# Optimization experiments

Measured on AMD Instinct MI355X. Metric: run time of the kernel, lower is better.

Reference implementation:

```python
import jax, jax.numpy as jnp
import numpy as np
from jax import lax

DIM = 64
NUM_EXPERTS = 6
TOP_K = 2
B, H, W = 8, 128, 128
DN = ('NCHW', 'OIHW', 'NCHW')


def setup_inputs() -> dict:
    key = jax.random.key(0)
    ks = jax.random.split(key, 8)
    s_in = 1.0 / np.sqrt(DIM * 9)
    s_r = 1.0 / np.sqrt(DIM)
    return {
        'x': jax.random.normal(ks[0], (B, DIM, H, W), jnp.float32),
        'router_w': jax.random.normal(ks[1], (NUM_EXPERTS, DIM), jnp.float32) * s_r,
        'router_b': jnp.zeros((NUM_EXPERTS,), jnp.float32),
        'expert_bias': jnp.zeros((NUM_EXPERTS,), jnp.float32),
        'w1': jax.random.normal(ks[2], (NUM_EXPERTS, DIM, DIM, 3, 3), jnp.float32) * s_in,
        'b1': jnp.zeros((NUM_EXPERTS, DIM), jnp.float32),
        'w2': jax.random.normal(ks[3], (NUM_EXPERTS, DIM, DIM, 3, 3), jnp.float32) * s_in,
        'b2': jnp.zeros((NUM_EXPERTS, DIM), jnp.float32),
    }


def reference(x, router_w, router_b, expert_bias, w1, b1, w2, b2):
    # ---- router: global avg pool -> linear -> clamp -> +bias -> softmax ----
    pooled = x.mean(axis=(2, 3))                               # [B, C]
    logits = pooled @ router_w.T + router_b                    # [B, E]
    logits = jnp.clip(logits, -10.0, 10.0) + expert_bias[None, :]
    probs = jnp.clip(jax.nn.softmax(logits, axis=1), 1e-6, 1.0)
    top_v, top_i = lax.top_k(probs, TOP_K)                     # [B, K]
    top_v = top_v / (top_v.sum(axis=1, keepdims=True) + 1e-8)
    # per-sample combine weight for each expert: sum of top-k probs routed to it
    w_be = (jax.nn.one_hot(top_i, NUM_EXPERTS, dtype=x.dtype) * top_v[..., None]).sum(axis=1)  # [B, E]

    # ---- experts: Conv3x3 -> GELU -> Conv3x3, vmapped over expert dim ----
    def expert(w1e, b1e, w2e, b2e):
        h = lax.conv_general_dilated(x, w1e, (1, 1), 'SAME', dimension_numbers=DN)
        h = jax.nn.gelu(h + b1e[None, :, None, None])
        h = lax.conv_general_dilated(h, w2e, (1, 1), 'SAME', dimension_numbers=DN)
        return h + b2e[None, :, None, None]

    ys = jax.vmap(expert)(w1, b1, w2, b2)                      # [E, B, C, H, W]
    out = jnp.einsum('be,ebchw->bchw', w_be, ys)
    return out, jnp.zeros((), x.dtype)
```

## Files before the change

kernel.cpp:

```cpp
#include <hip/hip_runtime.h>
#include <hip/hip_bf16.h>
#include <cstdint>

typedef __attribute__((ext_vector_type(8))) short sh8;
typedef __attribute__((ext_vector_type(16))) float f32x16;
typedef unsigned short ushort_t;

#define HH 128
#define WW 128
#define HWSZ (HH*WW)
#define PW 130
#define PW64 (PW*64)
#define IMGSZ ((size_t)PW*PW*64)
#define WBEXP 36864

#define SCOLS 34
#define ROWB (SCOLS*128)
#define TRT 4
#define SRT 6
#define CHT (SRT*SCOLS*8)

typedef __attribute__((address_space(1))) const void gvoid_t;
typedef __attribute__((address_space(3))) void lvoid_t;

__device__ __forceinline__ float gelu_fast(float x) {
    float m = x * __builtin_fmaf(x * x, -0.10294323f, -2.30220805f);
    return x * __builtin_amdgcn_rcpf(1.0f + __builtin_amdgcn_exp2f(m));
}
__device__ __forceinline__ ushort_t f2b(float f) {
    __hip_bfloat16 h = __float2bfloat16(f);
    return *reinterpret_cast<ushort_t*>(&h);
}
__device__ __forceinline__ unsigned pack2(float a, float b) {
    return (unsigned)f2b(a) | ((unsigned)f2b(b) << 16);
}
__device__ __forceinline__ f32x16 mfma_bf16(sh8 a, sh8 b, f32x16 c) {
    return __builtin_amdgcn_mfma_f32_32x32x16_bf16(a, b, c, 0, 0, 0);
}

__device__ __forceinline__ void stage_gll(const ushort_t* __restrict__ imgRow,
                                          char* smem, int w0, int tid) {
#pragma unroll
    for (int it = 0; it < 7; ++it) {
        int idx = tid + it * 256;
        if (idx < CHT) {
            int row = idx / (SCOLS * 8);
            int rem = idx - row * (SCOLS * 8);
            int col = rem >> 3;
            int ch  = (rem & 7) ^ (col & 7);
            const ushort_t* src = imgRow + (size_t)row * PW64 + (size_t)(w0 + col) * 64 + ch * 8;
            __builtin_amdgcn_global_load_lds((gvoid_t*)src, (lvoid_t*)(smem + idx * 16),
                                             16, 0, 0);
        }
    }
}

__device__ __forceinline__ void conv_phase1(const char* sm, const ushort_t* wt_,
                                            int row, int l31, int lh,
                                            f32x16& acc0, f32x16& acc1, int dc) {
    sh8 wf[8];
#pragma unroll
    for (int kc = 0; kc < 4; ++kc) {
        wf[kc * 2]     = *reinterpret_cast<const sh8*>(wt_ + kc * 1024);
        wf[kc * 2 + 1] = *reinterpret_cast<const sh8*>(wt_ + kc * 1024 + 512);
    }
    __builtin_amdgcn_sched_barrier(0);
    const int colb = (dc + l31) * 128;
    const int swz = ((dc + l31) & 7) << 4;
#pragma unroll
    for (int kc = 0; kc < 4; ++kc) {
        sh8 a = *reinterpret_cast<const sh8*>(sm + row * ROWB + ((colb + (kc * 2 + lh) * 16) ^ swz));
        acc0 = mfma_bf16(wf[kc * 2], a, acc0);
        acc1 = mfma_bf16(wf[kc * 2 + 1], a, acc1);
    }
}

__global__ __launch_bounds__(64) void router_kernel(const float* __restrict__ pooled,
                                                    const float* __restrict__ rw,
                                                    const float* __restrict__ rb,
                                                    const float* __restrict__ eb,
                                                    const float* __restrict__ b2,
                                                    int* __restrict__ topi,
                                                    float* __restrict__ topw,
                                                    float* __restrict__ bsum,
                                                    float* __restrict__ outz) {
    __shared__ int sti[16];
    __shared__ float stw[16];
    int b = threadIdx.x;
    if (b == 8) outz[(size_t)8 * 64 * HWSZ] = 0.f;
    if (b < 8) {
        float lg[6];
        for (int e = 0; e < 6; ++e) {
            float s = 0.f;
            for (int c = 0; c < 64; ++c) s += pooled[b * 64 + c] * rw[e * 64 + c];
            s = s * (1.0f / (float)HWSZ) + rb[e];
            lg[e] = fminf(fmaxf(s, -10.f), 10.f) + eb[e];
        }
        float m = lg[0];
        for (int e = 1; e < 6; ++e) m = fmaxf(m, lg[e]);
        float den = 0.f, pr[6];
        for (int e = 0; e < 6; ++e) { pr[e] = expf(lg[e] - m); den += pr[e]; }
        float inv = 1.0f / den;
        for (int e = 0; e < 6; ++e) pr[e] = fminf(fmaxf(pr[e] * inv, 1e-6f), 1.0f);
        int i0 = 0; float v0 = pr[0];
        for (int e = 1; e < 6; ++e) if (pr[e] > v0) { v0 = pr[e]; i0 = e; }
        int i1 = -1; float v1 = -1.f;
        for (int e = 0; e < 6; ++e) { if (e == i0) continue; if (pr[e] > v1) { v1 = pr[e]; i1 = e; } }
        float s2 = v0 + v1 + 1e-8f;
        topi[b * 2 + 0] = i0; topi[b * 2 + 1] = i1;
        topw[b * 2 + 0] = v0 / s2; topw[b * 2 + 1] = v1 / s2;
        sti[b * 2 + 0] = i0; sti[b * 2 + 1] = i1;
        stw[b * 2 + 0] = v0 / s2; stw[b * 2 + 1] = v1 / s2;
    }
    __syncthreads();
    for (int i = threadIdx.x; i < 512; i += 64) {
        int bb = i >> 6, c = i & 63;
        bsum[i] = stw[bb * 2] * b2[sti[bb * 2] * 64 + c] +
                  stw[bb * 2 + 1] * b2[sti[bb * 2 + 1] * 64 + c];
    }
}

__global__ __launch_bounds__(256) void convx_kernel(const float* __restrict__ x,
                                                    ushort_t* __restrict__ xp,
                                                    float* __restrict__ pooled) {
    __shared__ ushort_t lt[128][72];
    int b = blockIdx.x >> 7, h = blockIdx.x & 127;
    int tid = threadIdx.x;
#pragma unroll
    for (int k = 0; k < 8; ++k) {
        int idx = tid + k * 256;
        int ci = idx >> 5, wg = idx & 31;
        float4 v = *reinterpret_cast<const float4*>(
            x + ((size_t)b * 64 + ci) * HWSZ + (size_t)h * WW + wg * 4);
        lt[wg * 4 + 0][ci] = f2b(v.x);
        lt[wg * 4 + 1][ci] = f2b(v.y);
        lt[wg * 4 + 2][ci] = f2b(v.z);
        lt[wg * 4 + 3][ci] = f2b(v.w);
        float s4 = (v.x + v.y) + (v.z + v.w);
#pragma unroll
        for (int m = 16; m > 0; m >>= 1) s4 += __shfl_xor(s4, m, 64);
        if ((tid & 31) == 0) atomicAdd(pooled + b * 64 + ci, s4);
    }
    __syncthreads();
    int w = tid >> 1, half = tid & 1;
    const int4* src = reinterpret_cast<const int4*>(&lt[w][half * 32]);
    int4 a0 = src[0], a1 = src[1], a2 = src[2], a3 = src[3];
    int4* dst = reinterpret_cast<int4*>(
        xp + (((size_t)b * PW + (h + 1)) * PW + (w + 1)) * 64 + half * 32);
    dst[0] = a0; dst[1] = a1; dst[2] = a2; dst[3] = a3;
}

__global__ __launch_bounds__(256) void prep_kernel(const float* __restrict__ w1,
                                                   const float* __restrict__ w2,
                                                   const int* __restrict__ topi,
                                                   const float* __restrict__ topw,
                                                   ushort_t* __restrict__ wb1f,
                                                   ushort_t* __restrict__ wb2f,
                                                   ushort_t* __restrict__ xp,
                                                   ushort_t* __restrict__ hp) {
    int blk = blockIdx.x;
    int tid = threadIdx.x;
    if (blk < 54) {
        int e = blk / 9, t = blk - e * 9;
        for (int idx = tid; idx < 4096; idx += 256) {
            int kc = idx >> 10, n = (idx >> 9) & 1, l = (idx >> 3) & 63, j = idx & 7;
            int co = n * 32 + (l & 31);
            int ci = kc * 16 + (l >> 5) * 8 + j;
            wb1f[(size_t)e * WBEXP + t * 4096 + idx] =
                f2b(w1[(((size_t)e * 64 + co) * 64 + ci) * 9 + t]);
        }
    } else if (blk < 198) {
        int q = blk - 54;
        int bs = q / 9, t = q - bs * 9;
        int e = topi[bs];
        float cw = topw[bs];
        for (int idx = tid; idx < 4096; idx += 256) {
            int kc = idx >> 10, n = (idx >> 9) & 1, l = (idx >> 3) & 63, j = idx & 7;
            int co = n * 32 + (l & 31);
            int ci = kc * 16 + (l >> 5) * 8 + j;
            wb2f[(size_t)bs * WBEXP + t * 4096 + idx] =
                f2b(cw * w2[(((size_t)e * 64 + co) * 64 + ci) * 9 + t]);
        }
    } else {
        int img = blk - 198;
        ushort_t* p = (img < 8) ? (xp + (size_t)img * IMGSZ)
                                : (hp + (size_t)(img - 8) * IMGSZ);
        int4 z = make_int4(0, 0, 0, 0);
        for (int i = tid; i < 1040; i += 256) {
            reinterpret_cast<int4*>(p)[i] = z;
            reinterpret_cast<int4*>(p + (size_t)129 * PW64)[i] = z;
        }
        for (int i = tid; i < 128 * 8; i += 256) {
            int row = 1 + (i >> 3), j = i & 7;
            reinterpret_cast<int4*>(p + (size_t)row * PW64)[j] = z;
            reinterpret_cast<int4*>(p + ((size_t)row * PW + 129) * 64)[j] = z;
        }
    }
}

__global__ __launch_bounds__(256) void conv1_mfma(const ushort_t* __restrict__ xp,
                                                  const ushort_t* __restrict__ wb1f,
                                                  const float* __restrict__ b1,
                                                  const int* __restrict__ topi,
                                                  ushort_t* __restrict__ hp,
                                                  int nslots, int slot0) {
    __shared__ char smem[CHT * 16];
    const int z = blockIdx.z;
    const int b = z / nslots, sl = z - b * nslots, s = slot0 + sl;
    const int e = topi[b * 2 + s];
    const int tid = threadIdx.x, l = tid & 63, wid = tid >> 6;
    const int l31 = l & 31, lh = l >> 5;
    const int ht = blockIdx.x >> 2, wt = blockIdx.x & 3;
    const int h0 = ht * TRT, w0 = wt * 32;
    const int row0 = wid;

    stage_gll(xp + (size_t)b * IMGSZ + (size_t)h0 * PW64, smem, w0, tid);

    const ushort_t* wB = wb1f + (size_t)e * WBEXP + l * 8;
    f32x16 acc0, acc1;
#pragma unroll
    for (int k2 = 0; k2 < 16; ++k2) { acc0[k2] = 0.f; acc1[k2] = 0.f; }
    __syncthreads();

#pragma unroll
    for (int dr = 0; dr < 3; ++dr)
#pragma unroll
        for (int dc = 0; dc < 3; ++dc)
            conv_phase1(smem, wB + (dr * 3 + dc) * 4096, row0 + dr, l31, lh, acc0, acc1, dc);

    float4 bq[2][4];
#pragma unroll
    for (int n = 0; n < 2; ++n)
#pragma unroll
        for (int g = 0; g < 4; ++g)
            bq[n][g] = *reinterpret_cast<const float4*>(b1 + e * 64 + n * 32 + g * 8 + 4 * lh);
    const size_t pbase = (size_t)(sl * 8 + b) * IMGSZ +
                         (size_t)(h0 + row0 + 1) * PW64 + (size_t)(w0 + l31 + 1) * 64;
#pragma unroll
    for (int n = 0; n < 2; ++n) {
        f32x16 a = n ? acc1 : acc0;
#pragma unroll
        for (int g = 0; g < 4; ++g) {
            float v0 = gelu_fast(a[g * 4 + 0] + bq[n][g].x);
            float v1 = gelu_fast(a[g * 4 + 1] + bq[n][g].y);
            float v2 = gelu_fast(a[g * 4 + 2] + bq[n][g].z);
            float v3 = gelu_fast(a[g * 4 + 3] + bq[n][g].w);
            uint2 u; u.x = pack2(v0, v1); u.y = pack2(v2, v3);
            *reinterpret_cast<uint2*>(hp + pbase + n * 32 + g * 8 + 4 * lh) = u;
        }
    }
}

template <int NS>
__global__ __launch_bounds__(256) void conv2_mfma(const ushort_t* __restrict__ hp,
                                                  const ushort_t* __restrict__ wb2f,
                                                  const float* __restrict__ bsum,
                                                  float* __restrict__ outF,
                                                  int s0, int addmode) {
    __shared__ char smem[2][CHT * 16];
    const int b = blockIdx.z;
    const int tid = threadIdx.x, l = tid & 63, wid = tid >> 6;
    const int l31 = l & 31, lh = l >> 5;
    const int ht = blockIdx.x >> 2, wt = blockIdx.x & 3;
    const int h0 = ht * TRT, w0 = wt * 32;
    const int row0 = wid;

    stage_gll(hp + (size_t)b * IMGSZ + (size_t)h0 * PW64, smem[0], w0, tid);

    f32x16 acc0, acc1;
#pragma unroll
    for (int k2 = 0; k2 < 16; ++k2) { acc0[k2] = 0.f; acc1[k2] = 0.f; }
    __syncthreads();

    if (NS == 2)
        stage_gll(hp + (size_t)(8 + b) * IMGSZ + (size_t)h0 * PW64, smem[1], w0, tid);

    {
        const ushort_t* wB = wb2f + (size_t)(b * 2 + s0) * WBEXP + l * 8;
#pragma unroll
        for (int dr = 0; dr < 3; ++dr)
#pragma unroll
            for (int dc = 0; dc < 3; ++dc)
                conv_phase1(smem[0], wB + (dr * 3 + dc) * 4096, row0 + dr, l31, lh, acc0, acc1, dc);
    }
    if (NS == 2) {
        __syncthreads();
        const ushort_t* wB = wb2f + (size_t)(b * 2 + s0 + 1) * WBEXP + l * 8;
#pragma unroll
        for (int dr = 0; dr < 3; ++dr)
#pragma unroll
            for (int dc = 0; dc < 3; ++dc)
                conv_phase1(smem[1], wB + (dr * 3 + dc) * 4096, row0 + dr, l31, lh, acc0, acc1, dc);
    }

    __syncthreads();
    float* lt = reinterpret_cast<float*>(smem[0]) + wid * 1056;
    float4 bq[2][4];
#pragma unroll
    for (int n = 0; n < 2; ++n)
#pragma unroll
        for (int g = 0; g < 4; ++g)
            bq[n][g] = addmode ? make_float4(0.f, 0.f, 0.f, 0.f)
                               : *reinterpret_cast<const float4*>(bsum + b * 64 + n * 32 + g * 8 + 4 * lh);
    const int h = h0 + row0;
#pragma unroll
    for (int n = 0; n < 2; ++n) {
        f32x16 a = n ? acc1 : acc0;
#pragma unroll
        for (int r = 0; r < 16; ++r) {
            int co = (r & 3) + 8 * (r >> 2) + 4 * lh;
            float bv = (r & 3) == 0 ? bq[n][r >> 2].x : (r & 3) == 1 ? bq[n][r >> 2].y
                     : (r & 3) == 2 ? bq[n][r >> 2].z : bq[n][r >> 2].w;
            lt[l31 * 33 + co] = a[r] + bv;
        }
        const int q = lh, co = l31;
        const size_t ob = ((size_t)(b * 64 + n * 32 + co)) * HWSZ + (size_t)h * WW + w0 + q * 16;
#pragma unroll
        for (int v = 0; v < 4; ++v) {
            float o0 = lt[(q * 16 + v * 4 + 0) * 33 + co];
            float o1 = lt[(q * 16 + v * 4 + 1) * 33 + co];
            float o2 = lt[(q * 16 + v * 4 + 2) * 33 + co];
            float o3 = lt[(q * 16 + v * 4 + 3) * 33 + co];
            float4* dst = reinterpret_cast<float4*>(outF + ob + v * 4);
            if (addmode) {
                float4 pv = *dst;
                o0 += pv.x; o1 += pv.y; o2 += pv.z; o3 += pv.w;
            }
            float4 o; o.x = o0; o.y = o1; o.z = o2; o.w = o3;
            *dst = o;
        }
    }
}

extern "C" void kernel_launch(void* const* d_in, const int* in_sizes, int n_in,
                              void* d_out, int out_size, void* d_ws, size_t ws_size,
                              hipStream_t stream) {
    const float* x  = (const float*)d_in[0];
    const float* rw = (const float*)d_in[1];
    const float* rb = (const float*)d_in[2];
    const float* eb = (const float*)d_in[3];
    const float* w1 = (const float*)d_in[4];
    const float* b1 = (const float*)d_in[5];
    const float* w2 = (const float*)d_in[6];
    const float* b2 = (const float*)d_in[7];
    float* out = (float*)d_out;

    char* ws = (char*)d_ws;
    float*    pooled = (float*)(ws + 0);
    int*      topi   = (int*)(ws + 2048);
    float*    topw   = (float*)(ws + 2112);
    float*    bsum   = (float*)(ws + 2176);
    ushort_t* wb1f   = (ushort_t*)(ws + 4352);
    ushort_t* wb2f   = (ushort_t*)(ws + 446720);
    ushort_t* xp     = (ushort_t*)(ws + 1626368);
    ushort_t* hp     = (ushort_t*)(ws + 18931968);

    const bool two = ws_size >= 53543168ull;

    hipMemsetAsync(pooled, 0, 512 * sizeof(float), stream);
    hipLaunchKernelGGL(convx_kernel, dim3(1024), dim3(256), 0, stream, x, xp, pooled);
    hipLaunchKernelGGL(router_kernel, dim3(1), dim3(64), 0, stream,
                       pooled, rw, rb, eb, b2, topi, topw, bsum, out);
    hipLaunchKernelGGL(prep_kernel, dim3(198 + 8 + (two ? 16 : 8)), dim3(256), 0, stream,
                       w1, w2, topi, topw, wb1f, wb2f, xp, hp);

    if (two) {
        hipLaunchKernelGGL(conv1_mfma, dim3(128, 1, 16), dim3(256), 0, stream,
                           xp, wb1f, b1, topi, hp, 2, 0);
        hipLaunchKernelGGL((conv2_mfma<2>), dim3(128, 1, 8), dim3(256), 0, stream,
                           hp, wb2f, bsum, out, 0, 0);
    } else {
        hipLaunchKernelGGL(conv1_mfma, dim3(128, 1, 8), dim3(256), 0, stream,
                           xp, wb1f, b1, topi, hp, 1, 0);
        hipLaunchKernelGGL((conv2_mfma<1>), dim3(128, 1, 8), dim3(256), 0, stream,
                           hp, wb2f, bsum, out, 0, 0);
        hipLaunchKernelGGL(conv1_mfma, dim3(128, 1, 8), dim3(256), 0, stream,
                           xp, wb1f, b1, topi, hp, 1, 1);
        hipLaunchKernelGGL((conv2_mfma<1>), dim3(128, 1, 8), dim3(256), 0, stream,
                           hp, wb2f, bsum, out, 1, 1);
    }
}
```

Baseline: 211.2 us.

## Halve conv tile rows and split output channels across waves

Each block now covers 2 output rows instead of 4, and each wave computes one 32-channel half of the output instead of both halves. This doubles the grid and cuts per-wave accumulator registers and LDS footprint, which should raise occupancy. The two-slot conv2 now reuses a single LDS buffer and restages sequentially with extra barriers, which drops the earlier prefetch overlap. Smaller tiles also increase halo reload overhead, since each block now loads 4 staged rows for 2 output rows rather than 6 for 4.

```diff
diff --git a/kernel.cpp b/kernel.cpp
--- a/kernel.cpp
+++ b/kernel.cpp
@@ -16,8 +16,8 @@
 
 #define SCOLS 34
 #define ROWB (SCOLS*128)
-#define TRT 4
-#define SRT 6
+#define TRT 2
+#define SRT 4
 #define CHT (SRT*SCOLS*8)
 
 typedef __attribute__((address_space(1))) const void gvoid_t;
@@ -41,7 +41,7 @@
 __device__ __forceinline__ void stage_gll(const ushort_t* __restrict__ imgRow,
                                           char* smem, int w0, int tid) {
 #pragma unroll
-    for (int it = 0; it < 7; ++it) {
+    for (int it = 0; it < 5; ++it) {
         int idx = tid + it * 256;
         if (idx < CHT) {
             int row = idx / (SCOLS * 8);
@@ -57,21 +57,18 @@
 
 __device__ __forceinline__ void conv_phase1(const char* sm, const ushort_t* wt_,
                                             int row, int l31, int lh,
-                                            f32x16& acc0, f32x16& acc1, int dc) {
-    sh8 wf[8];
-#pragma unroll
-    for (int kc = 0; kc < 4; ++kc) {
-        wf[kc * 2]     = *reinterpret_cast<const sh8*>(wt_ + kc * 1024);
-        wf[kc * 2 + 1] = *reinterpret_cast<const sh8*>(wt_ + kc * 1024 + 512);
-    }
+                                            f32x16& acc, int dc) {
+    sh8 wf[4];
+#pragma unroll
+    for (int kc = 0; kc < 4; ++kc)
+        wf[kc] = *reinterpret_cast<const sh8*>(wt_ + kc * 1024);
     __builtin_amdgcn_sched_barrier(0);
     const int colb = (dc + l31) * 128;
     const int swz = ((dc + l31) & 7) << 4;
 #pragma unroll
     for (int kc = 0; kc < 4; ++kc) {
         sh8 a = *reinterpret_cast<const sh8*>(sm + row * ROWB + ((colb + (kc * 2 + lh) * 16) ^ swz));
-        acc0 = mfma_bf16(wf[kc * 2], a, acc0);
-        acc1 = mfma_bf16(wf[kc * 2 + 1], a, acc1);
+        acc = mfma_bf16(wf[kc], a, acc);
     }
 }
 
@@ -212,42 +209,37 @@
     const int l31 = l & 31, lh = l >> 5;
     const int ht = blockIdx.x >> 2, wt = blockIdx.x & 3;
     const int h0 = ht * TRT, w0 = wt * 32;
-    const int row0 = wid;
+    const int row0 = wid >> 1;
+    const int n = wid & 1;
 
     stage_gll(xp + (size_t)b * IMGSZ + (size_t)h0 * PW64, smem, w0, tid);
 
-    const ushort_t* wB = wb1f + (size_t)e * WBEXP + l * 8;
-    f32x16 acc0, acc1;
-#pragma unroll
-    for (int k2 = 0; k2 < 16; ++k2) { acc0[k2] = 0.f; acc1[k2] = 0.f; }
+    const ushort_t* wB = wb1f + (size_t)e * WBEXP + n * 512 + l * 8;
+    f32x16 acc;
+#pragma unroll
+    for (int k2 = 0; k2 < 16; ++k2) acc[k2] = 0.f;
     __syncthreads();
 
 #pragma unroll
     for (int dr = 0; dr < 3; ++dr)
 #pragma unroll
         for (int dc = 0; dc < 3; ++dc)
-            conv_phase1(smem, wB + (dr * 3 + dc) * 4096, row0 + dr, l31, lh, acc0, acc1, dc);
-
-    float4 bq[2][4];
-#pragma unroll
-    for (int n = 0; n < 2; ++n)
-#pragma unroll
-        for (int g = 0; g < 4; ++g)
-            bq[n][g] = *reinterpret_cast<const float4*>(b1 + e * 64 + n * 32 + g * 8 + 4 * lh);
+            conv_phase1(smem, wB + (dr * 3 + dc) * 4096, row0 + dr, l31, lh, acc, dc);
+
+    float4 bq[4];
+#pragma unroll
+    for (int g = 0; g < 4; ++g)
+        bq[g] = *reinterpret_cast<const float4*>(b1 + e * 64 + n * 32 + g * 8 + 4 * lh);
     const size_t pbase = (size_t)(sl * 8 + b) * IMGSZ +
                          (size_t)(h0 + row0 + 1) * PW64 + (size_t)(w0 + l31 + 1) * 64;
 #pragma unroll
-    for (int n = 0; n < 2; ++n) {
-        f32x16 a = n ? acc1 : acc0;
-#pragma unroll
-        for (int g = 0; g < 4; ++g) {
-            float v0 = gelu_fast(a[g * 4 + 0] + bq[n][g].x);
-            float v1 = gelu_fast(a[g * 4 + 1] + bq[n][g].y);
-            float v2 = gelu_fast(a[g * 4 + 2] + bq[n][g].z);
-            float v3 = gelu_fast(a[g * 4 + 3] + bq[n][g].w);
-            uint2 u; u.x = pack2(v0, v1); u.y = pack2(v2, v3);
-            *reinterpret_cast<uint2*>(hp + pbase + n * 32 + g * 8 + 4 * lh) = u;
-        }
+    for (int g = 0; g < 4; ++g) {
+        float v0 = gelu_fast(acc[g * 4 + 0] + bq[g].x);
+        float v1 = gelu_fast(acc[g * 4 + 1] + bq[g].y);
+        float v2 = gelu_fast(acc[g * 4 + 2] + bq[g].z);
+        float v3 = gelu_fast(acc[g * 4 + 3] + bq[g].w);
+        uint2 u; u.x = pack2(v0, v1); u.y = pack2(v2, v3);
+        *reinterpret_cast<uint2*>(hp + pbase + n * 32 + g * 8 + 4 * lh) = u;
     }
 }
 
@@ -257,78 +249,72 @@
                                                   const float* __restrict__ bsum,
                                                   float* __restrict__ outF,
                                                   int s0, int addmode) {
-    __shared__ char smem[2][CHT * 16];
+    __shared__ char smem[CHT * 16];
     const int b = blockIdx.z;
     const int tid = threadIdx.x, l = tid & 63, wid = tid >> 6;
     const int l31 = l & 31, lh = l >> 5;
     const int ht = blockIdx.x >> 2, wt = blockIdx.x & 3;
     const int h0 = ht * TRT, w0 = wt * 32;
-    const int row0 = wid;
-
-    stage_gll(hp + (size_t)b * IMGSZ + (size_t)h0 * PW64, smem[0], w0, tid);
-
-    f32x16 acc0, acc1;
-#pragma unroll
-    for (int k2 = 0; k2 < 16; ++k2) { acc0[k2] = 0.f; acc1[k2] = 0.f; }
-    __syncthreads();
-
-    if (NS == 2)
-        stage_gll(hp + (size_t)(8 + b) * IMGSZ + (size_t)h0 * PW64, smem[1], w0, tid);
+    const int row0 = wid >> 1;
+    const int n = wid & 1;
+
+    stage_gll(hp + (size_t)b * IMGSZ + (size_t)h0 * PW64, smem, w0, tid);
+
+    f32x16 acc;
+#pragma unroll
+    for (int k2 = 0; k2 < 16; ++k2) acc[k2] = 0.f;
+    __syncthreads();
 
     {
-        const ushort_t* wB = wb2f + (size_t)(b * 2 + s0) * WBEXP + l * 8;
+        const ushort_t* wB = wb2f + (size_t)(b * 2 + s0) * WBEXP + n * 512 + l * 8;
 #pragma unroll
         for (int dr = 0; dr < 3; ++dr)
 #pragma unroll
             for (int dc = 0; dc < 3; ++dc)
-                conv_phase1(smem[0], wB + (dr * 3 + dc) * 4096, row0 + dr, l31, lh, acc0, acc1, dc);
+                conv_phase1(smem, wB + (dr * 3 + dc) * 4096, row0 + dr, l31, lh, acc, dc);
     }
     if (NS == 2) {
         __syncthreads();
-        const ushort_t* wB = wb2f + (size_t)(b * 2 + s0 + 1) * WBEXP + l * 8;
+        stage_gll(hp + (size_t)(8 + b) * IMGSZ + (size_t)h0 * PW64, smem, w0, tid);
+        __syncthreads();
+        const ushort_t* wB = wb2f + (size_t)(b * 2 + s0 + 1) * WBEXP + n * 512 + l * 8;
 #pragma unroll
         for (int dr = 0; dr < 3; ++dr)
 #pragma unroll
             for (int dc = 0; dc < 3; ++dc)
-                conv_phase1(smem[1], wB + (dr * 3 + dc) * 4096, row0 + dr, l31, lh, acc0, acc1, dc);
-    }
-
-    __syncthreads();
-    float* lt = reinterpret_cast<float*>(smem[0]) + wid * 1056;
-    float4 bq[2][4];
-#pragma unroll
-    for (int n = 0; n < 2; ++n)
-#pragma unroll
-        for (int g = 0; g < 4; ++g)
-            bq[n][g] = addmode ? make_float4(0.f, 0.f, 0.f, 0.f)
-                               : *reinterpret_cast<const float4*>(bsum + b * 64 + n * 32 + g * 8 + 4 * lh);
+                conv_phase1(smem, wB + (dr * 3 + dc) * 4096, row0 + dr, l31, lh, acc, dc);
+    }
+
+    __syncthreads();
+    float* lt = reinterpret_cast<float*>(smem) + wid * 1056;
+    float4 bq[4];
+#pragma unroll
+    for (int g = 0; g < 4; ++g)
+        bq[g] = addmode ? make_float4(0.f, 0.f, 0.f, 0.f)
+                        : *reinterpret_cast<const float4*>(bsum + b * 64 + n * 32 + g * 8 + 4 * lh);
     const int h = h0 + row0;
 #pragma unroll
-    for (int n = 0; n < 2; ++n) {
-        f32x16 a = n ? acc1 : acc0;
-#pragma unroll
-        for (int r = 0; r < 16; ++r) {
-            int co = (r & 3) + 8 * (r >> 2) + 4 * lh;
-            float bv = (r & 3) == 0 ? bq[n][r >> 2].x : (r & 3) == 1 ? bq[n][r >> 2].y
-                     : (r & 3) == 2 ? bq[n][r >> 2].z : bq[n][r >> 2].w;
-            lt[l31 * 33 + co] = a[r] + bv;
-        }
-        const int q = lh, co = l31;
-        const size_t ob = ((size_t)(b * 64 + n * 32 + co)) * HWSZ + (size_t)h * WW + w0 + q * 16;
-#pragma unroll
-        for (int v = 0; v < 4; ++v) {
-            float o0 = lt[(q * 16 + v * 4 + 0) * 33 + co];
-            float o1 = lt[(q * 16 + v * 4 + 1) * 33 + co];
-            float o2 = lt[(q * 16 + v * 4 + 2) * 33 + co];
-            float o3 = lt[(q * 16 + v * 4 + 3) * 33 + co];
-            float4* dst = reinterpret_cast<float4*>(outF + ob + v * 4);
-            if (addmode) {
-                float4 pv = *dst;
-                o0 += pv.x; o1 += pv.y; o2 += pv.z; o3 += pv.w;
-            }
-            float4 o; o.x = o0; o.y = o1; o.z = o2; o.w = o3;
-            *dst = o;
-        }
+    for (int r = 0; r < 16; ++r) {
+        int co = (r & 3) + 8 * (r >> 2) + 4 * lh;
+        float bv = (r & 3) == 0 ? bq[r >> 2].x : (r & 3) == 1 ? bq[r >> 2].y
+                 : (r & 3) == 2 ? bq[r >> 2].z : bq[r >> 2].w;
+        lt[l31 * 33 + co] = acc[r] + bv;
+    }
+    const int q = lh, co = l31;
+    const size_t ob = ((size_t)(b * 64 + n * 32 + co)) * HWSZ + (size_t)h * WW + w0 + q * 16;
+#pragma unroll
+    for (int v = 0; v < 4; ++v) {
+        float o0 = lt[(q * 16 + v * 4 + 0) * 33 + co];
+        float o1 = lt[(q * 16 + v * 4 + 1) * 33 + co];
+        float o2 = lt[(q * 16 + v * 4 + 2) * 33 + co];
+        float o3 = lt[(q * 16 + v * 4 + 3) * 33 + co];
+        float4* dst = reinterpret_cast<float4*>(outF + ob + v * 4);
+        if (addmode) {
+            float4 pv = *dst;
+            o0 += pv.x; o1 += pv.y; o2 += pv.z; o3 += pv.w;
+        }
+        float4 o; o.x = o0; o.y = o1; o.z = o2; o.w = o3;
+        *dst = o;
     }
 }
 
@@ -365,18 +351,18 @@
                        w1, w2, topi, topw, wb1f, wb2f, xp, hp);
 
     if (two) {
-        hipLaunchKernelGGL(conv1_mfma, dim3(128, 1, 16), dim3(256), 0, stream,
+        hipLaunchKernelGGL(conv1_mfma, dim3(256, 1, 16), dim3(256), 0, stream,
                            xp, wb1f, b1, topi, hp, 2, 0);
-        hipLaunchKernelGGL((conv2_mfma<2>), dim3(128, 1, 8), dim3(256), 0, stream,
+        hipLaunchKernelGGL((conv2_mfma<2>), dim3(256, 1, 8), dim3(256), 0, stream,
                            hp, wb2f, bsum, out, 0, 0);
     } else {
-        hipLaunchKernelGGL(conv1_mfma, dim3(128, 1, 8), dim3(256), 0, stream,
+        hipLaunchKernelGGL(conv1_mfma, dim3(256, 1, 8), dim3(256), 0, stream,
                            xp, wb1f, b1, topi, hp, 1, 0);
-        hipLaunchKernelGGL((conv2_mfma<1>), dim3(128, 1, 8), dim3(256), 0, stream,
+        hipLaunchKernelGGL((conv2_mfma<1>), dim3(256, 1, 8), dim3(256), 0, stream,
                            hp, wb2f, bsum, out, 0, 0);
-        hipLaunchKernelGGL(conv1_mfma, dim3(128, 1, 8), dim3(256), 0, stream,
+        hipLaunchKernelGGL(conv1_mfma, dim3(256, 1, 8), dim3(256), 0, stream,
                            xp, wb1f, b1, topi, hp, 1, 1);
-        hipLaunchKernelGGL((conv2_mfma<1>), dim3(128, 1, 8), dim3(256), 0, stream,
+        hipLaunchKernelGGL((conv2_mfma<1>), dim3(256, 1, 8), dim3(256), 0, stream,
                            hp, wb2f, bsum, out, 1, 1);
     }
 }
```

New measurement: 222.1 us. 5.2% more time.
